# Kernel tuning notes

Measured on AMD Instinct MI355X. Metric: run time of the kernel, lower is better.

Reference implementation:

```python
import jax, jax.numpy as jnp
import numpy as np

N = 50000      # nodes
E = 800000     # edges (avg degree 16)
LM = 768       # lm_input_dim
H = 192        # hidden_dim = 32*6
B6 = 32        # per-branch dim = hidden_dim/6
SLOPE = 0.01   # nn.LeakyReLU default negative slope


def setup_inputs() -> dict:
    key = jax.random.key(0)
    ks = jax.random.split(key, 32)
    f = lambda i, shape, s=0.05: (jax.random.normal(ks[i], shape, jnp.float32) * s)
    inp = {
        "pre_x": f(0, (N, LM)),
        "x": f(1, (N, LM)),
        "edge_index": jax.random.randint(ks[2], (2, E), 0, N),
        "edge_type": jax.random.randint(ks[3], (E,), 0, 3),
        "num_prop": f(4, (N, 5)),
        "num_category": f(5, (N, 1)),
        "des_tensor": f(6, (N, LM)),
        "tweet_tensor": f(7, (N, LM)),
        # parameters (torch nn.Linear convention: W is [out, in], y = x @ W.T + b)
        "W_des": f(8, (B6, LM)), "b_des": f(9, (B6,)),
        "W_tweet": f(10, (B6, LM)), "b_tweet": f(11, (B6,)),
        "W_tweet_tr": f(12, (B6, LM)), "b_tweet_tr": f(13, (B6,)),
        "W_prop": f(14, (B6, 5)), "b_prop": f(15, (B6,)),
        "W_cat": f(16, (B6, 1)), "b_cat": f(17, (B6,)),
        "W_text": f(18, (B6, LM)), "b_text": f(19, (B6,)),
        "W_in": f(20, (H, H)), "b_in": f(21, (H,)),
        "W_c1": f(22, (H, H)), "b_c1": f(23, (H,)),
        "W_c2": f(24, (H, H)), "b_c2": f(25, (H,)),
        "W_o1": f(26, (96, H)), "b_o1": f(27, (96,)),
        "W_o2": f(28, (2, 96)), "b_o2": f(29, (2,)),
    }
    return inp


def _gcn_conv(h, W, b, src, dst):
    """PyG GCNConv: symmetric-normalized aggregation with added self-loops.
    out[v] = sum_{u->v} (d_u d_v)^{-1/2} (h_u W^T) + (1/d_v) (h_v W^T) + b
    where d includes the self-loop (+1)."""
    n = h.shape[0]
    hW = h @ W.T                                                  # [N, H]
    deg = jax.ops.segment_sum(jnp.ones(src.shape[0], h.dtype), dst,
                              num_segments=n) + 1.0               # [N]
    dinv = jax.lax.rsqrt(deg)
    norm = dinv[src] * dinv[dst]                                  # [E]
    agg = jax.ops.segment_sum(hW[src] * norm[:, None], dst,
                              num_segments=n)                     # [N, H]
    return agg + hW * (1.0 / deg)[:, None] + b


def reference(pre_x, x, edge_index, edge_type, num_prop, num_category,
              des_tensor, tweet_tensor,
              W_des, b_des, W_tweet, b_tweet, W_tweet_tr, b_tweet_tr,
              W_prop, b_prop, W_cat, b_cat, W_text, b_text,
              W_in, b_in, W_c1, b_c1, W_c2, b_c2,
              W_o1, b_o1, W_o2, b_o2):
    lrelu = lambda v: jax.nn.leaky_relu(v, SLOPE)
    branch = lambda t, W, b: lrelu(t @ W.T + b)   # dropout is identity in eval

    d = branch(des_tensor, W_des, b_des)
    pre_t = branch(pre_x, W_tweet, b_tweet)
    t = branch(x, W_tweet_tr, b_tweet_tr)
    n = branch(num_prop, W_prop, b_prop)
    c = branch(num_category, W_cat, b_cat)
    tw = branch(tweet_tensor, W_text, b_text)

    h = jnp.concatenate((n, c, d, tw, pre_t, t), axis=1)          # [N, 192]
    h = lrelu(h @ W_in.T + b_in)

    src, dst = edge_index[0], edge_index[1]
    h = _gcn_conv(h, W_c1, b_c1, src, dst)
    h = _gcn_conv(h, W_c2, b_c2, src, dst)

    em = lrelu(h @ W_o1.T + b_o1)                                 # [N, 96]
    out = em @ W_o2.T + b_o2                                      # [N, 2]
    return (out, em)
```

## Files before the change

### kernel.cpp

```cpp
#include <hip/hip_runtime.h>

#define NN 50000
#define EE 800000
#define LMD 768
#define HD 192
#define SLOPE 0.01f

typedef short bf16x8 __attribute__((ext_vector_type(8)));
typedef float f32x4 __attribute__((ext_vector_type(4)));
typedef unsigned short u16;

__device__ __forceinline__ float lrelu(float v){ return v > 0.f ? v : SLOPE * v; }

__device__ __forceinline__ u16 f2bf(float f){
    unsigned u = __float_as_uint(f);
    u += 0x7FFF + ((u >> 16) & 1u);
    return (u16)(u >> 16);
}
__device__ __forceinline__ float bf2f(u16 v){
    return __uint_as_float(((unsigned)v) << 16);
}
__device__ __forceinline__ bf16x8 as_bf8(float4 v){
    union { float4 f; bf16x8 b; } u; u.f = v; return u.b;
}

__global__ __launch_bounds__(256) void k_prep(
    const float* __restrict__ W0, const float* __restrict__ W1,
    const float* __restrict__ W2, const float* __restrict__ W3,
    const float* __restrict__ Win, const float* __restrict__ Wc1,
    const float* __restrict__ Wc2, const float* __restrict__ Wo1,
    u16* __restrict__ out)
{
    int m = blockIdx.y;
    int idx = blockIdx.x * 256 + threadIdx.x;
    const float* src; int nelem; int K;
    switch (m) {
      case 0: src = W0;  nelem = 32*768;  K = 768; break;
      case 1: src = W1;  nelem = 32*768;  K = 768; break;
      case 2: src = W2;  nelem = 32*768;  K = 768; break;
      case 3: src = W3;  nelem = 32*768;  K = 768; break;
      case 4: src = Win; nelem = 192*192; K = 192; break;
      case 5: src = Wc1; nelem = 192*192; K = 192; break;
      case 6: src = Wc2; nelem = 192*192; K = 192; break;
      default: src = Wo1; nelem = 96*192; K = 192; break;
    }
    if (idx >= nelem) return;
    u16 v = f2bf(src[idx]);
    int c = idx / K, k = idx - c * K;
    int cb = c >> 4, lr = c & 15;
    int sg = k >> 5, kk = k & 31, hi = kk >> 3, j = kk & 7;
    int lane = hi * 16 + lr;
    size_t dst;
    if (m < 4)      dst = (size_t)m * 24576 + (sg * 2 + cb) * 512 + lane * 8 + j;
    else if (m < 7) dst = 98304 + (size_t)(m - 4) * 36864 + (sg * 12 + cb) * 512 + lane * 8 + j;
    else            dst = 208896 + (size_t)(sg * 6 + cb) * 512 + lane * 8 + j;
    out[dst] = v;
}

__global__ __launch_bounds__(256, 3) void k_branch(
    const float* __restrict__ des, const float* __restrict__ twt,
    const float* __restrict__ prex, const float* __restrict__ xx,
    const u16* __restrict__ Wf,
    const float* __restrict__ bd, const float* __restrict__ btx,
    const float* __restrict__ btw, const float* __restrict__ btr,
    u16* __restrict__ h,
    const int* __restrict__ ei, int* __restrict__ deg)
{
    __shared__ u16 Abuf[16][776];
    __shared__ float scr[4][16][32];

    if (blockIdx.x >= 192) {
        int rid = blockIdx.y * 64 + (blockIdx.x - 192);
        for (int e = rid * 256 + threadIdx.x; e < EE; e += 65536)
            atomicAdd(&deg[ei[EE + e]], 1);
        return;
    }

    const int br = blockIdx.y;
    const float* A; const float* bias; int colBase;
    switch (br) {
      case 0:  A = des;  bias = bd;  colBase = 64;  break;
      case 1:  A = twt;  bias = btx; colBase = 96;  break;
      case 2:  A = prex; bias = btw; colBase = 128; break;
      default: A = xx;   bias = btr; colBase = 160; break;
    }

    const int t0 = threadIdx.x, w = t0 >> 6, l = t0 & 63;
    const int hi = l >> 4, lr = l & 15;

    bf16x8 Bfr[12];
    {
        const u16* wp = Wf + br * 24576;
        #pragma unroll
        for (int cc = 0; cc < 6; ++cc)
            #pragma unroll
            for (int cb = 0; cb < 2; ++cb)
                Bfr[cc * 2 + cb] = *(const bf16x8*)(wp + ((w * 6 + cc) * 2 + cb) * 512 + l * 8);
    }

    const int rrow = t0 >> 4;
    const int col0 = (t0 & 15) * 2;
    const float bias0 = bias[col0], bias1 = bias[col0 + 1];

    float4 f4[12];
    int tile = blockIdx.x;
    {
        const float* ab = A + (size_t)tile * 12288 + w * 3072 + l * 4;
        #pragma unroll
        for (int i = 0; i < 12; ++i) f4[i] = *(const float4*)(ab + i * 256);
    }

    for (; tile < 3125; tile += 192) {
        asm volatile("s_waitcnt vmcnt(0)" ::: "memory");
        #pragma unroll
        for (int i = 0; i < 12; ++i) {
            const int rr = i / 3, third = i % 3;
            uint2 pk;
            pk.x = (unsigned)f2bf(f4[i].x) | ((unsigned)f2bf(f4[i].y) << 16);
            pk.y = (unsigned)f2bf(f4[i].z) | ((unsigned)f2bf(f4[i].w) << 16);
            *(uint2*)&Abuf[w * 4 + rr][third * 256 + l * 4] = pk;
        }
        const int tnext = tile + 192;
        if (tnext < 3125) {
            const float* ab = A + (size_t)tnext * 12288 + w * 3072 + l * 4;
            #pragma unroll
            for (int i = 0; i < 12; ++i) f4[i] = *(const float4*)(ab + i * 256);
        }
        __syncthreads();

        f32x4 acc[2] = {};
        #pragma unroll
        for (int cc = 0; cc < 6; ++cc) {
            const int cg = w * 6 + cc;
            bf16x8 af = *(const bf16x8*)&Abuf[lr][cg * 32 + hi * 8];
            acc[0] = __builtin_amdgcn_mfma_f32_16x16x32_bf16(af, Bfr[cc * 2 + 0], acc[0], 0, 0, 0);
            acc[1] = __builtin_amdgcn_mfma_f32_16x16x32_bf16(af, Bfr[cc * 2 + 1], acc[1], 0, 0, 0);
        }
        #pragma unroll
        for (int cb = 0; cb < 2; ++cb)
            #pragma unroll
            for (int rg = 0; rg < 4; ++rg)
                scr[w][hi * 4 + rg][cb * 16 + lr] = acc[cb][rg];
        __syncthreads();

        float2 s; s.x = 0.f; s.y = 0.f;
        #pragma unroll
        for (int ww = 0; ww < 4; ++ww) {
            float2 p = *(const float2*)&scr[ww][rrow][col0];
            s.x += p.x; s.y += p.y;
        }
        unsigned pk = (unsigned)f2bf(lrelu(s.x + bias0)) | ((unsigned)f2bf(lrelu(s.y + bias1)) << 16);
        *(unsigned*)&h[((size_t)tile * 16 + rrow) * HD + colBase + col0] = pk;
    }
}

__global__ __launch_bounds__(256) void k_small_scan(
    const float* __restrict__ nprop, const float* __restrict__ ncat,
    const float* __restrict__ Wp, const float* __restrict__ bp,
    const float* __restrict__ Wc, const float* __restrict__ bc,
    u16* __restrict__ h,
    const int* __restrict__ deg, int* __restrict__ rp, int* __restrict__ part,
    float* __restrict__ dinv, float* __restrict__ invdeg)
{
    if (blockIdx.x >= 1563) {
        __shared__ int sh[256];
        int sb = blockIdx.x - 1563;
        int tid = threadIdx.x;
        int i = sb * 256 + tid;
        int x = (i < NN) ? deg[i] : 0;
        if (i < NN) {
            float d = (float)(x + 1);
            dinv[i] = rsqrtf(d);
            invdeg[i] = 1.0f / d;
        }
        sh[tid] = x;
        __syncthreads();
        for (int off = 1; off < 256; off <<= 1) {
            int y = (tid >= off) ? sh[tid - off] : 0;
            __syncthreads();
            sh[tid] += y;
            __syncthreads();
        }
        if (i < NN) rp[i] = sh[tid] - x;
        if (tid == 255) part[sb] = sh[255];
        return;
    }

    __shared__ float sWp[160], sbp[32], sWc[32], sbc[32];
    int t = threadIdx.x;
    if (t < 160) sWp[t] = Wp[t];
    else if (t < 192) sbp[t - 160] = bp[t - 160];
    else if (t < 224) sWc[t - 192] = Wc[t - 192];
    else              sbc[t - 224] = bc[t - 224];
    __syncthreads();

    int idx = blockIdx.x * 256 + t;
    if (idx >= NN * 8) return;
    int row = idx >> 3, g = idx & 7;
    float o[8];
    if (g < 4) {
        float np[5];
        #pragma unroll
        for (int k = 0; k < 5; ++k) np[k] = nprop[row * 5 + k];
        #pragma unroll
        for (int j = 0; j < 8; ++j) {
            int c = g * 8 + j;
            float a = sbp[c];
            #pragma unroll
            for (int k = 0; k < 5; ++k) a += np[k] * sWp[c * 5 + k];
            o[j] = lrelu(a);
        }
    } else {
        float nc = ncat[row];
        #pragma unroll
        for (int j = 0; j < 8; ++j) {
            int cc = (g - 4) * 8 + j;
            o[j] = lrelu(sbc[cc] + nc * sWc[cc]);
        }
    }
    uint4 pk;
    pk.x = (unsigned)f2bf(o[0]) | ((unsigned)f2bf(o[1]) << 16);
    pk.y = (unsigned)f2bf(o[2]) | ((unsigned)f2bf(o[3]) << 16);
    pk.z = (unsigned)f2bf(o[4]) | ((unsigned)f2bf(o[5]) << 16);
    pk.w = (unsigned)f2bf(o[6]) | ((unsigned)f2bf(o[7]) << 16);
    *(uint4*)&h[(size_t)row * HD + g * 8] = pk;
}

template<bool BIAS, bool LRELU, int ROLE>
__global__ __launch_bounds__(512) void k_hgemm(
    const u16* __restrict__ A, const u16* __restrict__ Wf,
    const float* __restrict__ bias, u16* __restrict__ out,
    const int* __restrict__ deg, int* __restrict__ rp, const int* __restrict__ part,
    int* __restrict__ cursor, const int* __restrict__ ei,
    int* __restrict__ cs, float* __restrict__ nrm, const float* __restrict__ dinv)
{
    __shared__ u16 Bs[36864];
    if (ROLE == 1 && blockIdx.x >= 391) {
        int sb = blockIdx.x - 391;
        int tid = threadIdx.x;
        if (tid < 256) {
            int pre = 0;
            for (int j = 0; j < sb; ++j) pre += part[j];
            int i = sb * 256 + tid;
            if (i < NN) {
                int v = rp[i] + pre;
                rp[i] = v;
                cursor[i] = v;
                if (i == NN - 1) rp[NN] = v + deg[i];
            }
        }
        return;
    }
    if (ROLE == 2 && blockIdx.x >= 391) {
        int rid = blockIdx.x - 391;
        for (int e = rid * 512 + threadIdx.x; e < EE; e += 102400) {
            int s = ei[e], d = ei[EE + e];
            int pos = atomicAdd(&cursor[d], 1);
            cs[pos] = s;
            nrm[pos] = dinv[s] * dinv[d];
        }
        return;
    }

    const int t = threadIdx.x, w = t >> 6, l = t & 63;
    const int hi = l >> 4, lr = l & 15;
    const int rowBase = blockIdx.x * 128;
    {
        const uint4* s_ = (const uint4*)Wf; uint4* d_ = (uint4*)Bs;
        #pragma unroll
        for (int i = 0; i < 9; ++i) d_[i * 512 + t] = s_[i * 512 + t];
    }
    int r0 = rowBase + w * 16 + lr;
    int rowc = r0 < NN ? r0 : NN - 1;
    const u16* ap = A + (size_t)rowc * HD;
    float4 araw[6];
    #pragma unroll
    for (int sg = 0; sg < 6; ++sg) {
        araw[sg] = *(const float4*)(ap + sg * 32 + hi * 8);
        asm volatile("" :: "v"(araw[sg].x), "v"(araw[sg].y), "v"(araw[sg].z), "v"(araw[sg].w));
    }
    __syncthreads();

    f32x4 acc[12] = {};
    #pragma unroll
    for (int sg = 0; sg < 6; ++sg) {
        bf16x8 af = as_bf8(araw[sg]);
        #pragma unroll
        for (int cb = 0; cb < 12; ++cb) {
            bf16x8 bf = *(const bf16x8*)(Bs + (sg * 12 + cb) * 512 + l * 8);
            acc[cb] = __builtin_amdgcn_mfma_f32_16x16x32_bf16(af, bf, acc[cb], 0, 0, 0);
        }
    }

    #pragma unroll
    for (int cb = 0; cb < 12; ++cb) {
        int cl = cb * 16 + lr;
        float bv = BIAS ? bias[cl] : 0.f;
        #pragma unroll
        for (int rg = 0; rg < 4; ++rg) {
            int r = rowBase + w * 16 + hi * 4 + rg;
            if (r < NN) {
                float v = acc[cb][rg] + bv;
                if (LRELU) v = lrelu(v);
                out[(size_t)r * HD + cl] = f2bf(v);
            }
        }
    }
}

__global__ __launch_bounds__(512) void k_final(
    const u16* __restrict__ A, const u16* __restrict__ Wf,
    const float* __restrict__ b1, const float* __restrict__ W2,
    const float* __restrict__ b2, float* __restrict__ em, float* __restrict__ out)
{
    __shared__ u16 Bs[18432];
    const int t = threadIdx.x, w = t >> 6, l = t & 63;
    const int hi = l >> 4, lr = l & 15;
    const int rowBase = blockIdx.x * 128;
    {
        const uint4* s_ = (const uint4*)Wf; uint4* d_ = (uint4*)Bs;
        #pragma unroll
        for (int i = 0; i < 5; ++i) { int idx = i * 512 + t; if (idx < 2304) d_[idx] = s_[idx]; }
    }
    int r0 = rowBase + w * 16 + lr;
    int rowc = r0 < NN ? r0 : NN - 1;
    const u16* ap = A + (size_t)rowc * HD;
    float4 araw[6];
    #pragma unroll
    for (int sg = 0; sg < 6; ++sg) {
        araw[sg] = *(const float4*)(ap + sg * 32 + hi * 8);
        asm volatile("" :: "v"(araw[sg].x), "v"(araw[sg].y), "v"(araw[sg].z), "v"(araw[sg].w));
    }
    __syncthreads();

    f32x4 acc[6] = {};
    #pragma unroll
    for (int sg = 0; sg < 6; ++sg) {
        bf16x8 af = as_bf8(araw[sg]);
        #pragma unroll
        for (int cb = 0; cb < 6; ++cb) {
            bf16x8 bf = *(const bf16x8*)(Bs + (sg * 6 + cb) * 512 + l * 8);
            acc[cb] = __builtin_amdgcn_mfma_f32_16x16x32_bf16(af, bf, acc[cb], 0, 0, 0);
        }
    }

    float w2v[2][6], bv[6];
    #pragma unroll
    for (int cb = 0; cb < 6; ++cb) {
        bv[cb] = b1[cb * 16 + lr];
        w2v[0][cb] = W2[cb * 16 + lr];
        w2v[1][cb] = W2[96 + cb * 16 + lr];
    }

    #pragma unroll
    for (int rg = 0; rg < 4; ++rg) {
        int r = rowBase + w * 16 + hi * 4 + rg;
        float o0 = 0.f, o1 = 0.f;
        #pragma unroll
        for (int cb = 0; cb < 6; ++cb) {
            float v = lrelu(acc[cb][rg] + bv[cb]);
            if (r < NN) em[(size_t)r * 96 + cb * 16 + lr] = v;
            o0 += v * w2v[0][cb];
            o1 += v * w2v[1][cb];
        }
        #pragma unroll
        for (int d = 1; d < 16; d <<= 1) {
            o0 += __shfl_xor(o0, d);
            o1 += __shfl_xor(o1, d);
        }
        if (lr == 0 && r < NN) {
            out[r * 2 + 0] = o0 + b2[0];
            out[r * 2 + 1] = o1 + b2[1];
        }
    }
}

__global__ __launch_bounds__(256) void k_agg(const u16* __restrict__ hW,
    const int* __restrict__ rp, const int* __restrict__ cs, const float* __restrict__ nrm,
    const float* __restrict__ invdeg, const float* __restrict__ bias, u16* __restrict__ out)
{
    int lane = threadIdx.x;
    if (lane >= 48) return;
    int v = blockIdx.x * 4 + threadIdx.y;
    int f0 = lane * 4;
    int s0 = rp[v], s1 = rp[v + 1];
    float4 bv = *reinterpret_cast<const float4*>(bias + f0);
    ushort4 hv = *reinterpret_cast<const ushort4*>(hW + (size_t)v * HD + f0);
    float idg = invdeg[v];
    float a0 = bf2f(hv.x) * idg + bv.x;
    float a1 = bf2f(hv.y) * idg + bv.y;
    float a2 = bf2f(hv.z) * idg + bv.z;
    float a3 = bf2f(hv.w) * idg + bv.w;
    int i = s0;
    for (; i + 8 <= s1; i += 8) {
        int c[8]; float n[8]; ushort4 g[8];
        #pragma unroll
        for (int j = 0; j < 8; ++j) { c[j] = cs[i + j]; n[j] = nrm[i + j]; }
        #pragma unroll
        for (int j = 0; j < 8; ++j)
            g[j] = *reinterpret_cast<const ushort4*>(hW + (size_t)c[j] * HD + f0);
        #pragma unroll
        for (int j = 0; j < 8; ++j) {
            a0 += bf2f(g[j].x) * n[j]; a1 += bf2f(g[j].y) * n[j];
            a2 += bf2f(g[j].z) * n[j]; a3 += bf2f(g[j].w) * n[j];
        }
    }
    for (; i < s1; ++i) {
        int c = cs[i]; float n = nrm[i];
        ushort4 g = *reinterpret_cast<const ushort4*>(hW + (size_t)c * HD + f0);
        a0 += bf2f(g.x) * n; a1 += bf2f(g.y) * n; a2 += bf2f(g.z) * n; a3 += bf2f(g.w) * n;
    }
    ushort4 o;
    o.x = f2bf(a0); o.y = f2bf(a1); o.z = f2bf(a2); o.w = f2bf(a3);
    *reinterpret_cast<ushort4*>(out + (size_t)v * HD + f0) = o;
}

extern "C" void kernel_launch(void* const* d_in, const int* in_sizes, int n_in,
                              void* d_out, int out_size, void* d_ws, size_t ws_size,
                              hipStream_t stream)
{
    const float* pre_x = (const float*)d_in[0];
    const float* x     = (const float*)d_in[1];
    const int*   ei    = (const int*)d_in[2];
    const float* nprop = (const float*)d_in[4];
    const float* ncat  = (const float*)d_in[5];
    const float* des   = (const float*)d_in[6];
    const float* twt   = (const float*)d_in[7];
    const float* W_des  = (const float*)d_in[8],  *b_des  = (const float*)d_in[9];
    const float* W_tw   = (const float*)d_in[10], *b_tw   = (const float*)d_in[11];
    const float* W_tr   = (const float*)d_in[12], *b_tr   = (const float*)d_in[13];
    const float* W_prop = (const float*)d_in[14], *b_prop = (const float*)d_in[15];
    const float* W_cat  = (const float*)d_in[16], *b_cat  = (const float*)d_in[17];
    const float* W_text = (const float*)d_in[18], *b_text = (const float*)d_in[19];
    const float* W_in   = (const float*)d_in[20], *b_in   = (const float*)d_in[21];
    const float* W_c1   = (const float*)d_in[22], *b_c1   = (const float*)d_in[23];
    const float* W_c2   = (const float*)d_in[24], *b_c2   = (const float*)d_in[25];
    const float* W_o1   = (const float*)d_in[26], *b_o1   = (const float*)d_in[27];
    const float* W_o2   = (const float*)d_in[28], *b_o2   = (const float*)d_in[29];

    char* base = (char*)d_ws;
    size_t off = 0;
    auto alloc = [&](size_t bytes) -> char* {
        char* p = base + off;
        off = (off + bytes + 255) & ~(size_t)255;
        return p;
    };
    u16*   hA     = (u16*)alloc((size_t)NN * HD * 2);
    u16*   hB     = (u16*)alloc((size_t)NN * HD * 2);
    u16*   hC     = (u16*)alloc((size_t)NN * HD * 2);
    u16*   Wprep  = (u16*)alloc((size_t)227328 * 2);
    float* dinv   = (float*)alloc((size_t)NN * 4);
    float* invdeg = (float*)alloc((size_t)NN * 4);
    int*   deg    = (int*)alloc((size_t)NN * 4);
    int*   rp     = (int*)alloc((size_t)(NN + 1) * 4);
    int*   cursor = (int*)alloc((size_t)NN * 4);
    int*   part   = (int*)alloc(256 * 4);
    int*   cs     = (int*)alloc((size_t)EE * 4);
    float* nrm    = (float*)alloc((size_t)EE * 4);
    (void)ws_size; (void)in_sizes; (void)n_in; (void)out_size;

    float* outp = (float*)d_out;
    float* em   = outp + (size_t)NN * 2;

    hipMemsetAsync(deg, 0, (size_t)NN * 4, stream);
    hipLaunchKernelGGL(k_prep, dim3(144, 8), dim3(256), 0, stream,
        W_des, W_text, W_tw, W_tr, W_in, W_c1, W_c2, W_o1, Wprep);

    hipLaunchKernelGGL(k_branch, dim3(256, 4), dim3(256), 0, stream,
        des, twt, pre_x, x, Wprep, b_des, b_text, b_tw, b_tr, hA, ei, deg);

    hipLaunchKernelGGL(k_small_scan, dim3(1759), dim3(256), 0, stream,
        nprop, ncat, W_prop, b_prop, W_cat, b_cat, hA,
        deg, rp, part, dinv, invdeg);

    hipLaunchKernelGGL((k_hgemm<true, true, 1>), dim3(587), dim3(512), 0, stream,
        hA, Wprep + 98304, b_in, hB,
        deg, rp, part, cursor, ei, cs, nrm, dinv);

    hipLaunchKernelGGL((k_hgemm<false, false, 2>), dim3(591), dim3(512), 0, stream,
        hB, Wprep + 98304 + 36864, nullptr, hC,
        deg, rp, part, cursor, ei, cs, nrm, dinv);

    hipLaunchKernelGGL(k_agg, dim3(NN / 4), dim3(64, 4), 0, stream,
        hC, rp, cs, nrm, invdeg, b_c1, hB);

    hipLaunchKernelGGL((k_hgemm<false, false, 0>), dim3(391), dim3(512), 0, stream,
        hB, Wprep + 98304 + 2 * 36864, nullptr, hC,
        deg, rp, part, cursor, ei, cs, nrm, dinv);

    hipLaunchKernelGGL(k_agg, dim3(NN / 4), dim3(64, 4), 0, stream,
        hC, rp, cs, nrm, invdeg, b_c2, hB);

    hipLaunchKernelGGL(k_final, dim3(391), dim3(512), 0, stream,
        hB, Wprep + 208896, b_o1, W_o2, b_o2, em, outp);
}
```

Before: 369.9 us.

## Fuse GCN aggregation with following GEMMs into per-tile kernels

Merges each GCN neighbor aggregation with the next dense matmul: a block aggregates 16 nodes into a swizzled LDS tile, then runs MFMA against weight fragments held in registers. The second aggregation is likewise fused with the output MLP (em and logits), with partial logits reduced through shared memory. This drops two kernel launches and the global round-trip of the aggregated features. In exchange each block reloads its weight fragments and only 16 rows are processed per block.

```diff
diff --git a/kernel.cpp b/kernel.cpp
--- a/kernel.cpp
+++ b/kernel.cpp
@@ -308,89 +308,19 @@
     }
 }
 
-__global__ __launch_bounds__(512) void k_final(
-    const u16* __restrict__ A, const u16* __restrict__ Wf,
-    const float* __restrict__ b1, const float* __restrict__ W2,
-    const float* __restrict__ b2, float* __restrict__ em, float* __restrict__ out)
-{
-    __shared__ u16 Bs[18432];
-    const int t = threadIdx.x, w = t >> 6, l = t & 63;
-    const int hi = l >> 4, lr = l & 15;
-    const int rowBase = blockIdx.x * 128;
-    {
-        const uint4* s_ = (const uint4*)Wf; uint4* d_ = (uint4*)Bs;
-        #pragma unroll
-        for (int i = 0; i < 5; ++i) { int idx = i * 512 + t; if (idx < 2304) d_[idx] = s_[idx]; }
-    }
-    int r0 = rowBase + w * 16 + lr;
-    int rowc = r0 < NN ? r0 : NN - 1;
-    const u16* ap = A + (size_t)rowc * HD;
-    float4 araw[6];
-    #pragma unroll
-    for (int sg = 0; sg < 6; ++sg) {
-        araw[sg] = *(const float4*)(ap + sg * 32 + hi * 8);
-        asm volatile("" :: "v"(araw[sg].x), "v"(araw[sg].y), "v"(araw[sg].z), "v"(araw[sg].w));
-    }
-    __syncthreads();
-
-    f32x4 acc[6] = {};
-    #pragma unroll
-    for (int sg = 0; sg < 6; ++sg) {
-        bf16x8 af = as_bf8(araw[sg]);
-        #pragma unroll
-        for (int cb = 0; cb < 6; ++cb) {
-            bf16x8 bf = *(const bf16x8*)(Bs + (sg * 6 + cb) * 512 + l * 8);
-            acc[cb] = __builtin_amdgcn_mfma_f32_16x16x32_bf16(af, bf, acc[cb], 0, 0, 0);
-        }
-    }
-
-    float w2v[2][6], bv[6];
-    #pragma unroll
-    for (int cb = 0; cb < 6; ++cb) {
-        bv[cb] = b1[cb * 16 + lr];
-        w2v[0][cb] = W2[cb * 16 + lr];
-        w2v[1][cb] = W2[96 + cb * 16 + lr];
-    }
-
-    #pragma unroll
-    for (int rg = 0; rg < 4; ++rg) {
-        int r = rowBase + w * 16 + hi * 4 + rg;
-        float o0 = 0.f, o1 = 0.f;
-        #pragma unroll
-        for (int cb = 0; cb < 6; ++cb) {
-            float v = lrelu(acc[cb][rg] + bv[cb]);
-            if (r < NN) em[(size_t)r * 96 + cb * 16 + lr] = v;
-            o0 += v * w2v[0][cb];
-            o1 += v * w2v[1][cb];
-        }
-        #pragma unroll
-        for (int d = 1; d < 16; d <<= 1) {
-            o0 += __shfl_xor(o0, d);
-            o1 += __shfl_xor(o1, d);
-        }
-        if (lr == 0 && r < NN) {
-            out[r * 2 + 0] = o0 + b2[0];
-            out[r * 2 + 1] = o1 + b2[1];
-        }
-    }
-}
-
-__global__ __launch_bounds__(256) void k_agg(const u16* __restrict__ hW,
+__device__ __forceinline__ void agg_node(const u16* __restrict__ hW,
     const int* __restrict__ rp, const int* __restrict__ cs, const float* __restrict__ nrm,
-    const float* __restrict__ invdeg, const float* __restrict__ bias, u16* __restrict__ out)
-{
-    int lane = threadIdx.x;
-    if (lane >= 48) return;
-    int v = blockIdx.x * 4 + threadIdx.y;
-    int f0 = lane * 4;
+    const float* __restrict__ invdeg, const float* __restrict__ bias,
+    int v, int f0, float& a0, float& a1, float& a2, float& a3)
+{
     int s0 = rp[v], s1 = rp[v + 1];
     float4 bv = *reinterpret_cast<const float4*>(bias + f0);
     ushort4 hv = *reinterpret_cast<const ushort4*>(hW + (size_t)v * HD + f0);
     float idg = invdeg[v];
-    float a0 = bf2f(hv.x) * idg + bv.x;
-    float a1 = bf2f(hv.y) * idg + bv.y;
-    float a2 = bf2f(hv.z) * idg + bv.z;
-    float a3 = bf2f(hv.w) * idg + bv.w;
+    a0 = bf2f(hv.x) * idg + bv.x;
+    a1 = bf2f(hv.y) * idg + bv.y;
+    a2 = bf2f(hv.z) * idg + bv.z;
+    a3 = bf2f(hv.w) * idg + bv.w;
     int i = s0;
     for (; i + 8 <= s1; i += 8) {
         int c[8]; float n[8]; ushort4 g[8];
@@ -410,9 +340,145 @@
         ushort4 g = *reinterpret_cast<const ushort4*>(hW + (size_t)c * HD + f0);
         a0 += bf2f(g.x) * n; a1 += bf2f(g.y) * n; a2 += bf2f(g.z) * n; a3 += bf2f(g.w) * n;
     }
-    ushort4 o;
-    o.x = f2bf(a0); o.y = f2bf(a1); o.z = f2bf(a2); o.w = f2bf(a3);
-    *reinterpret_cast<ushort4*>(out + (size_t)v * HD + f0) = o;
+}
+
+__global__ __launch_bounds__(256) void k_aggemm(const u16* __restrict__ hW,
+    const int* __restrict__ rp, const int* __restrict__ cs, const float* __restrict__ nrm,
+    const float* __restrict__ invdeg, const float* __restrict__ bias,
+    const u16* __restrict__ Wf, u16* __restrict__ out)
+{
+    __shared__ u16 tile[16 * 192];
+    const int lane = threadIdx.x, wv = threadIdx.y;
+    const int rowBase = blockIdx.x * 16;
+
+    bf16x8 Bfr[18];
+    #pragma unroll
+    for (int sg = 0; sg < 6; ++sg)
+        #pragma unroll
+        for (int c3 = 0; c3 < 3; ++c3)
+            Bfr[sg * 3 + c3] = *(const bf16x8*)(Wf + (sg * 12 + wv * 3 + c3) * 512 + lane * 8);
+
+    if (lane < 48) {
+        const int f0 = lane * 4;
+        const int chunk = f0 >> 3, within = f0 & 7;
+        for (int it = 0; it < 4; ++it) {
+            int rr = wv * 4 + it;
+            float a0, a1, a2, a3;
+            agg_node(hW, rp, cs, nrm, invdeg, bias, rowBase + rr, f0, a0, a1, a2, a3);
+            ushort4 o;
+            o.x = f2bf(a0); o.y = f2bf(a1); o.z = f2bf(a2); o.w = f2bf(a3);
+            *(ushort4*)&tile[rr * 192 + (chunk ^ (rr & 7)) * 8 + within] = o;
+        }
+    }
+    __syncthreads();
+
+    const int hi = lane >> 4, lr = lane & 15;
+    f32x4 acc[3] = {};
+    #pragma unroll
+    for (int sg = 0; sg < 6; ++sg) {
+        int ck = (sg * 4 + hi) ^ (lr & 7);
+        bf16x8 af = *(const bf16x8*)&tile[lr * 192 + ck * 8];
+        #pragma unroll
+        for (int c3 = 0; c3 < 3; ++c3)
+            acc[c3] = __builtin_amdgcn_mfma_f32_16x16x32_bf16(af, Bfr[sg * 3 + c3], acc[c3], 0, 0, 0);
+    }
+    #pragma unroll
+    for (int c3 = 0; c3 < 3; ++c3) {
+        int cl = (wv * 3 + c3) * 16 + lr;
+        #pragma unroll
+        for (int rg = 0; rg < 4; ++rg) {
+            int r = rowBase + hi * 4 + rg;
+            out[(size_t)r * HD + cl] = f2bf(acc[c3][rg]);
+        }
+    }
+}
+
+__global__ __launch_bounds__(256) void k_aggfinal(const u16* __restrict__ hW,
+    const int* __restrict__ rp, const int* __restrict__ cs, const float* __restrict__ nrm,
+    const float* __restrict__ invdeg, const float* __restrict__ bias,
+    const u16* __restrict__ Wf, const float* __restrict__ b1,
+    const float* __restrict__ W2, const float* __restrict__ b2,
+    float* __restrict__ em, float* __restrict__ outp)
+{
+    __shared__ u16 tile[16 * 192];
+    __shared__ float scrF[3][16][2];
+    const int lane = threadIdx.x, wv = threadIdx.y;
+    const int rowBase = blockIdx.x * 16;
+
+    bf16x8 Bfr[12];
+    if (wv < 3) {
+        #pragma unroll
+        for (int sg = 0; sg < 6; ++sg)
+            #pragma unroll
+            for (int ci = 0; ci < 2; ++ci)
+                Bfr[sg * 2 + ci] = *(const bf16x8*)(Wf + (sg * 6 + wv * 2 + ci) * 512 + lane * 8);
+    }
+
+    if (lane < 48) {
+        const int f0 = lane * 4;
+        const int chunk = f0 >> 3, within = f0 & 7;
+        for (int it = 0; it < 4; ++it) {
+            int rr = wv * 4 + it;
+            float a0, a1, a2, a3;
+            agg_node(hW, rp, cs, nrm, invdeg, bias, rowBase + rr, f0, a0, a1, a2, a3);
+            ushort4 o;
+            o.x = f2bf(a0); o.y = f2bf(a1); o.z = f2bf(a2); o.w = f2bf(a3);
+            *(ushort4*)&tile[rr * 192 + (chunk ^ (rr & 7)) * 8 + within] = o;
+        }
+    }
+    __syncthreads();
+
+    const int hi = lane >> 4, lr = lane & 15;
+    if (wv < 3) {
+        float w2v[2][2], bv1[2];
+        #pragma unroll
+        for (int ci = 0; ci < 2; ++ci) {
+            int cl = (wv * 2 + ci) * 16 + lr;
+            bv1[ci] = b1[cl];
+            w2v[0][ci] = W2[cl];
+            w2v[1][ci] = W2[96 + cl];
+        }
+        f32x4 acc[2] = {};
+        #pragma unroll
+        for (int sg = 0; sg < 6; ++sg) {
+            int ck = (sg * 4 + hi) ^ (lr & 7);
+            bf16x8 af = *(const bf16x8*)&tile[lr * 192 + ck * 8];
+            #pragma unroll
+            for (int ci = 0; ci < 2; ++ci)
+                acc[ci] = __builtin_amdgcn_mfma_f32_16x16x32_bf16(af, Bfr[sg * 2 + ci], acc[ci], 0, 0, 0);
+        }
+        #pragma unroll
+        for (int rg = 0; rg < 4; ++rg) {
+            int r = rowBase + hi * 4 + rg;
+            float o0 = 0.f, o1 = 0.f;
+            #pragma unroll
+            for (int ci = 0; ci < 2; ++ci) {
+                float v = lrelu(acc[ci][rg] + bv1[ci]);
+                em[(size_t)r * 96 + (wv * 2 + ci) * 16 + lr] = v;
+                o0 += v * w2v[0][ci];
+                o1 += v * w2v[1][ci];
+            }
+            #pragma unroll
+            for (int d = 1; d < 16; d <<= 1) {
+                o0 += __shfl_xor(o0, d);
+                o1 += __shfl_xor(o1, d);
+            }
+            if (lr == 0) {
+                scrF[wv][hi * 4 + rg][0] = o0;
+                scrF[wv][hi * 4 + rg][1] = o1;
+            }
+        }
+    }
+    __syncthreads();
+
+    int tid = wv * 64 + lane;
+    if (tid < 16) {
+        int r = rowBase + tid;
+        float o0 = scrF[0][tid][0] + scrF[1][tid][0] + scrF[2][tid][0] + b2[0];
+        float o1 = scrF[0][tid][1] + scrF[1][tid][1] + scrF[2][tid][1] + b2[1];
+        outp[r * 2 + 0] = o0;
+        outp[r * 2 + 1] = o1;
+    }
 }
 
 extern "C" void kernel_launch(void* const* d_in, const int* in_sizes, int n_in,
@@ -481,16 +547,9 @@
         hB, Wprep + 98304 + 36864, nullptr, hC,
         deg, rp, part, cursor, ei, cs, nrm, dinv);
 
-    hipLaunchKernelGGL(k_agg, dim3(NN / 4), dim3(64, 4), 0, stream,
-        hC, rp, cs, nrm, invdeg, b_c1, hB);
-
-    hipLaunchKernelGGL((k_hgemm<false, false, 0>), dim3(391), dim3(512), 0, stream,
-        hB, Wprep + 98304 + 2 * 36864, nullptr, hC,
-        deg, rp, part, cursor, ei, cs, nrm, dinv);
-
-    hipLaunchKernelGGL(k_agg, dim3(NN / 4), dim3(64, 4), 0, stream,
-        hC, rp, cs, nrm, invdeg, b_c2, hB);
-
-    hipLaunchKernelGGL(k_final, dim3(391), dim3(512), 0, stream,
-        hB, Wprep + 208896, b_o1, W_o2, b_o2, em, outp);
-}
+    hipLaunchKernelGGL(k_aggemm, dim3(NN / 16), dim3(64, 4), 0, stream,
+        hC, rp, cs, nrm, invdeg, b_c1, Wprep + 98304 + 2 * 36864, hA);
+
+    hipLaunchKernelGGL(k_aggfinal, dim3(NN / 16), dim3(64, 4), 0, stream,
+        hA, rp, cs, nrm, invdeg, b_c2, Wprep + 208896, b_o1, W_o2, b_o2, em, outp);
+}
```

After: 428.2 us. 1.16x slower.
